# Kernel tuning notes

Measured on AMD Instinct MI355X. Metric: run time of the kernel, lower is better.

Reference implementation:

```python
import jax, jax.numpy as jnp
import numpy as np

B = 4096
T_STEPS = 2048


def setup_inputs() -> dict:
    key = jax.random.key(0)
    k1, k2, k3 = jax.random.split(key, 3)
    inputs = jax.random.normal(k1, (B, T_STEPS), dtype=jnp.float32)
    # replicate torch init: params = rand(t); params /= sum(|params|); alternate signs
    p = jax.random.uniform(k2, (T_STEPS,), dtype=jnp.float32)
    p = p / jnp.sum(jnp.abs(p))
    sign = jnp.where(jnp.arange(T_STEPS) % 2 == 0, jnp.float32(1.0), jnp.float32(-1.0))
    params = p * sign
    bias = jax.random.normal(k3, (1,), dtype=jnp.float32)
    return {"inputs": inputs, "params": params, "bias": bias}


def reference(inputs, params, bias):
    """AR(t) recurrence: for i in [t, 2t): x_i = sum_j x_{i-1-j} * params[j] + bias.
    inputs: [B, t] seed values; returns the t generated values per row, [B, t].
    """
    t_steps = params.shape[0]
    # torch.dot uses inputs reversed (newest first) against params, so the
    # window kept in oldest->newest order pairs with reversed params.
    p_rev = params[::-1]

    def step(window, _):
        # window: [B, t] last t values, oldest -> newest
        new = window @ p_rev + bias[0]  # [B]
        window = jnp.concatenate([window[:, 1:], new[:, None]], axis=1)
        return window, new

    _, outs = jax.lax.scan(step, inputs, None, length=t_steps)
    return outs.T  # [B, t_steps]
```

## Files before the change

kernel.cpp:

```cpp
#include <hip/hip_runtime.h>
#include <hip/hip_bf16.h>

typedef _Float16 f16;
typedef _Float16 f16x8 __attribute__((ext_vector_type(8)));
typedef float f32x4 __attribute__((ext_vector_type(4)));

constexpr int TS = 2048;
constexpr int BB = 4096;

__device__ __forceinline__ int swz4(int c) { return c ^ ((c >> 3) & 7); }

struct ToepShared { char Xs[16384]; char Ws[8192]; };

union MegaShared {
  ToepShared t;
  struct {
    float rp1[2048];
    float h[2048];
    float hist[1024];
    float hbuf[2052];
  } hb;
};

template <bool REV>
__device__ void toep_body(ToepShared& lds, int w, const f16* __restrict__ Xg,
                          const char* __restrict__ Wg,
                          const float* __restrict__ biasp, void* __restrict__ Yg) {
  char* Xs = lds.Xs;
  char* Ws = lds.Ws;
  const int tid = threadIdx.x;
  const int lane = tid & 63;
  const int wid = tid >> 6;
  const int wrow = (wid >> 1) * 64;
  const int wcol = (wid & 1) * 32;
  const int px = w & 15;
  const int b0 = (w >> 4) * 128;

  float binit = 0.0f;
  if (REV) binit = biasp[0];

  for (int phase = 0; phase < 2; ++phase) {
    const int mblk = phase ? (31 - px) : px;
    const int m0 = mblk * 64;
    const int k0b = REV ? m0 : 0;
    const int k0e = REV ? TS : (m0 + 64);

    f32x4 acc[4][2];
    #pragma unroll
    for (int i = 0; i < 4; ++i)
      #pragma unroll
      for (int j = 0; j < 2; ++j) acc[i][j] = {binit, binit, binit, binit};

    for (int k0 = k0b; k0 < k0e; k0 += 64) {
      __syncthreads();
      #pragma unroll
      for (int t2 = 0; t2 < 4; ++t2) {
        const int t = wid * 4 + t2;
        const int row = t * 8 + (lane >> 3);
        const char* src = (const char*)Xg + ((size_t)(b0 + row) * TS + k0) * 2
                          + (((lane & 7) * 16) ^ ((row & 7) << 4));
        __builtin_amdgcn_global_load_lds(
            (const __attribute__((address_space(1))) unsigned int*)src,
            (__attribute__((address_space(3))) unsigned int*)(Xs + t * 1024),
            16, 0, 0);
      }
      const int dlt = (REV ? (k0 - m0) : (m0 - k0)) >> 6;
      const char* wsrc = Wg + (size_t)dlt * 8192;
      #pragma unroll
      for (int p = 0; p < 2; ++p) {
        const int t = wid * 2 + p;
        __builtin_amdgcn_global_load_lds(
            (const __attribute__((address_space(1))) unsigned int*)(wsrc + t * 1024 + lane * 16),
            (__attribute__((address_space(3))) unsigned int*)(Ws + t * 1024),
            16, 0, 0);
      }
      __syncthreads();

      #pragma unroll
      for (int ks = 0; ks < 2; ++ks) {
        const int colb = ks * 64 + ((lane >> 4) * 16);
        f16x8 af[4], bf[2];
        #pragma unroll
        for (int i = 0; i < 4; ++i) {
          const int row = wrow + i * 16 + (lane & 15);
          af[i] = *(const f16x8*)(Xs + row * 128 + (colb ^ ((row & 7) << 4)));
        }
        #pragma unroll
        for (int j = 0; j < 2; ++j) {
          const int n = wcol + j * 16 + (lane & 15);
          bf[j] = *(const f16x8*)(Ws + n * 128 + (colb ^ ((n & 7) << 4)));
        }
        #pragma unroll
        for (int i = 0; i < 4; ++i)
          #pragma unroll
          for (int j = 0; j < 2; ++j)
            acc[i][j] = __builtin_amdgcn_mfma_f32_16x16x32_f16(
                af[i], bf[j], acc[i][j], 0, 0, 0);
      }
    }

    #pragma unroll
    for (int i = 0; i < 4; ++i) {
      #pragma unroll
      for (int j = 0; j < 2; ++j) {
        #pragma unroll
        for (int r = 0; r < 4; ++r) {
          const int row = b0 + wrow + i * 16 + (lane >> 4) * 4 + r;
          const int col = m0 + wcol + j * 16 + (lane & 15);
          if (REV)
            ((f16*)Yg)[(size_t)row * TS + col] = (f16)acc[i][j][r];
          else
            ((float*)Yg)[(size_t)row * TS + col] = acc[i][j][r];
        }
      }
    }
  }
}

__device__ void h_block_body(MegaShared& lds, const float* __restrict__ params,
                             char* __restrict__ WgC) {
  float* rp1 = lds.hb.rp1;
  float* h_s = lds.hb.h;
  float* hist = lds.hb.hist;
  float* hb = lds.hb.hbuf;

  const int tid = threadIdx.x;
  const int lane = tid & 63;
  const int wave = tid >> 6;

  for (int c = tid; c < 512; c += 256) {
    const int y = c * 4;
    f32x4 v;
    v[0] = params[2046 - y];
    v[1] = params[2045 - y];
    v[2] = params[2044 - y];
    v[3] = (y + 3 < 2047) ? params[2043 - y] : 0.0f;
    *(f32x4*)&rp1[swz4(c) * 4] = v;
  }
  __syncthreads();

  if (wave == 0) {
    float hv = (lane == 0) ? 1.0f : 0.0f;
    for (int m = 1; m < 32; ++m) {
      float partial = 0.0f;
      if (lane < m) {
        const int yi = 2047 - m + lane;
        partial = hv * rp1[swz4(yi >> 2) * 4 + (yi & 3)];
      }
      #pragma unroll
      for (int off = 32; off; off >>= 1) partial += __shfl_xor(partial, off);
      if (lane == m) hv = partial;
    }
    if (lane < 32) h_s[lane] = hv;
  }
  __syncthreads();

  const int sub = tid & 7;
  const int g0 = tid >> 3;

  for (int n = 32; n < 2048; n <<= 1) {
    const int ng16 = n >> 4;
    const int T = (n >= 128) ? (n >> 7) : 1;

    for (int gi = g0; gi < ng16; gi += 32) {
      float acc[16];
      #pragma unroll
      for (int j = 0; j < 16; ++j) acc[j] = 0.0f;
      const int ybase = (2047 - n) - gi * 16 - 15;
      for (int t = 0; t < T; ++t) {
        const int m16 = (sub + 8 * t) * 16;
        if (m16 < n) {
          const int c0 = (ybase + m16) >> 2;
          f32x4 wv[8];
          #pragma unroll
          for (int q = 0; q < 8; ++q) wv[q] = *(const f32x4*)&rp1[swz4(c0 + q) * 4];
          f32x4 hv4[4];
          #pragma unroll
          for (int q = 0; q < 4; ++q) hv4[q] = *(const f32x4*)&h_s[m16 + 4 * q];
          #pragma unroll
          for (int d = 0; d < 16; ++d) {
            const float hd = hv4[d >> 2][d & 3];
            #pragma unroll
            for (int j = 0; j < 16; ++j) {
              const int k = d - j + 15;
              acc[j] += hd * wv[k >> 2][k & 3];
            }
          }
        }
      }
      #pragma unroll
      for (int j = 0; j < 16; ++j) {
        acc[j] += __shfl_xor(acc[j], 1);
        acc[j] += __shfl_xor(acc[j], 2);
        acc[j] += __shfl_xor(acc[j], 4);
      }
      if (sub == 0) {
        #pragma unroll
        for (int q = 0; q < 4; ++q) {
          f32x4 v = {acc[4 * q], acc[4 * q + 1], acc[4 * q + 2], acc[4 * q + 3]};
          *(f32x4*)&hist[gi * 16 + 4 * q] = v;
        }
      }
    }
    __syncthreads();

    const int P = n + 3;
    const int nchunk = (2 * n + 4) >> 2;
    for (int c = tid; c < nchunk; c += 256) {
      f32x4 v;
      #pragma unroll
      for (int q = 0; q < 4; ++q) {
        const int idx = 4 * c + q - P;
        v[q] = ((unsigned)idx < (unsigned)n) ? hist[idx] : 0.0f;
      }
      *(f32x4*)&hb[swz4(c) * 4] = v;
    }
    __syncthreads();

    for (int gi = g0; gi < ng16; gi += 32) {
      float acc[16];
      #pragma unroll
      for (int j = 0; j < 16; ++j) acc[j] = 0.0f;
      int t_end = (gi >= sub) ? (((gi - sub) >> 3) + 1) : 0;
      if (t_end > T) t_end = T;
      const int ybase = P + gi * 16 - 15;
      for (int t = 0; t < t_end; ++t) {
        const int r16 = (sub + 8 * t) * 16;
        const int c0 = (ybase - r16) >> 2;
        f32x4 wv[8];
        #pragma unroll
        for (int q = 0; q < 8; ++q) wv[q] = *(const f32x4*)&hb[swz4(c0 + q) * 4];
        f32x4 hv4[4];
        #pragma unroll
        for (int q = 0; q < 4; ++q) hv4[q] = *(const f32x4*)&h_s[r16 + 4 * q];
        #pragma unroll
        for (int d = 0; d < 16; ++d) {
          const float hd = hv4[d >> 2][d & 3];
          #pragma unroll
          for (int j = 0; j < 16; ++j) {
            const int k = j - d + 15;
            acc[j] += hd * wv[k >> 2][k & 3];
          }
        }
      }
      #pragma unroll
      for (int j = 0; j < 16; ++j) {
        acc[j] += __shfl_xor(acc[j], 1);
        acc[j] += __shfl_xor(acc[j], 2);
        acc[j] += __shfl_xor(acc[j], 4);
      }
      if (sub == 0) {
        #pragma unroll
        for (int q = 0; q < 4; ++q) {
          f32x4 v = {acc[4 * q], acc[4 * q + 1], acc[4 * q + 2], acc[4 * q + 3]};
          *(f32x4*)&h_s[n + gi * 16 + 4 * q] = v;
        }
      }
    }
    __syncthreads();
  }

  const int n2 = tid >> 2, kq = tid & 3;
  for (int dlt = 0; dlt < 32; ++dlt) {
    char* tile = WgC + (size_t)dlt * 8192;
    #pragma unroll
    for (int part = 0; part < 2; ++part) {
      const int k8 = kq * 16 + part * 8;
      f16x8 v;
      #pragma unroll
      for (int ii = 0; ii < 8; ++ii) {
        const int k = k8 + ii;
        const int dd = dlt * 64 + n2 - k;
        v[ii] = ((unsigned)dd < (unsigned)TS) ? (f16)h_s[dd] : (f16)0.0f;
      }
      *(f16x8*)(tile + n2 * 128 + ((2 * k8) ^ ((n2 & 7) << 4))) = v;
    }
  }
}

__global__ __launch_bounds__(256) void conv_prep(
    const float* __restrict__ X, f16* __restrict__ Xh,
    const float* __restrict__ params, char* __restrict__ Wg) {
  const int b = blockIdx.x;
  const int tid = threadIdx.x;
  if (b < 2048) {
    const size_t base = ((size_t)b * 256 + tid) * 16;
    const float4 a0 = *(const float4*)&X[base];
    const float4 a1 = *(const float4*)&X[base + 4];
    const float4 a2 = *(const float4*)&X[base + 8];
    const float4 a3 = *(const float4*)&X[base + 12];
    f16x8 v0 = {(f16)a0.x, (f16)a0.y, (f16)a0.z, (f16)a0.w,
                (f16)a1.x, (f16)a1.y, (f16)a1.z, (f16)a1.w};
    f16x8 v1 = {(f16)a2.x, (f16)a2.y, (f16)a2.z, (f16)a2.w,
                (f16)a3.x, (f16)a3.y, (f16)a3.z, (f16)a3.w};
    *(f16x8*)&Xh[base] = v0;
    *(f16x8*)&Xh[base + 8] = v1;
  } else {
    const int dlt = b - 2048;
    char* tile = Wg + (size_t)dlt * 8192;
    const int n = tid >> 2, kq = tid & 3;
    #pragma unroll
    for (int part = 0; part < 2; ++part) {
      const int k8 = kq * 16 + part * 8;
      f16x8 v;
      #pragma unroll
      for (int ii = 0; ii < 8; ++ii) {
        const int k = k8 + ii;
        const int dd = dlt * 64 + k - n;
        v[ii] = ((unsigned)dd < (unsigned)TS) ? (f16)params[2047 - dd] : (f16)0.0f;
      }
      *(f16x8*)(tile + n * 128 + ((2 * k8) ^ ((n & 7) << 4))) = v;
    }
  }
}

__global__ __launch_bounds__(256, 2) void mega_A(
    const f16* __restrict__ Xh, char* __restrict__ Wg,
    const float* __restrict__ biasp, f16* __restrict__ u,
    const float* __restrict__ params) {
  __shared__ MegaShared lds;
  const int b = blockIdx.x;
  if (b == 512) {
    h_block_body(lds, params, Wg + 32 * 8192);
    return;
  }
  toep_body<true>(lds.t, (b & 7) * 64 + (b >> 3), Xh, Wg, biasp, (void*)u);
}

__global__ __launch_bounds__(256, 2) void toep_C(
    const f16* __restrict__ u, const char* __restrict__ WgC,
    float* __restrict__ out) {
  __shared__ ToepShared lds;
  const int b = blockIdx.x;
  toep_body<false>(lds, (b & 7) * 64 + (b >> 3), u, WgC, nullptr, (void*)out);
}

extern "C" void kernel_launch(void* const* d_in, const int* in_sizes, int n_in,
                              void* d_out, int out_size, void* d_ws, size_t ws_size,
                              hipStream_t stream) {
  const float* inputs = (const float*)d_in[0];
  const float* params = (const float*)d_in[1];
  const float* bias   = (const float*)d_in[2];
  float* out = (float*)d_out;

  char* ws = (char*)d_ws;
  f16*  Xh = (f16*)ws;
  f16*  u  = (f16*)(ws + (size_t)BB * TS * 2);
  char* Wg = ws + (size_t)BB * TS * 4;

  conv_prep<<<2080, 256, 0, stream>>>(inputs, Xh, params, Wg);
  mega_A<<<513, 256, 0, stream>>>(Xh, Wg, bias, u, params);
  toep_C<<<512, 256, 0, stream>>>(u, Wg + 32 * 8192, out);
}
```

Before: 118.2 us.

## Move impulse-response block into prep kernel and halve per-thread output tile

The serial impulse-response (h) computation block moves from the first Toeplitz GEMM kernel into the conversion/prep kernel as block 0, so its long serial chain overlaps the bandwidth-bound fp32-to-fp16 conversion instead of extending the GEMM kernel's tail. The GEMM kernel no longer carries the large union shared-memory footprint. Inside the h block, each thread group now produces 8 outputs instead of 16, doubling the groups to spread work across more threads, and the h/hist arrays use swizzled LDS indexing to reduce bank conflicts. The cost is a prep kernel with a large static LDS allocation and launch bounds of 1, which may lower occupancy for the conversion blocks.

```diff
diff --git a/kernel.cpp b/kernel.cpp
--- a/kernel.cpp
+++ b/kernel.cpp
@@ -12,14 +12,11 @@
 
 struct ToepShared { char Xs[16384]; char Ws[8192]; };
 
-union MegaShared {
-  ToepShared t;
-  struct {
-    float rp1[2048];
-    float h[2048];
-    float hist[1024];
-    float hbuf[2052];
-  } hb;
+struct HShared {
+  float rp1[2048];
+  float h[2048];
+  float hist[1024];
+  float hbuf[2052];
 };
 
 template <bool REV>
@@ -117,12 +114,12 @@
   }
 }
 
-__device__ void h_block_body(MegaShared& lds, const float* __restrict__ params,
+__device__ void h_block_body(HShared& S, const float* __restrict__ params,
                              char* __restrict__ WgC) {
-  float* rp1 = lds.hb.rp1;
-  float* h_s = lds.hb.h;
-  float* hist = lds.hb.hist;
-  float* hb = lds.hb.hbuf;
+  float* rp1 = S.rp1;
+  float* h_s = S.h;
+  float* hist = S.hist;
+  float* hb = S.hbuf;
 
   const int tid = threadIdx.x;
   const int lane = tid & 63;
@@ -159,47 +156,46 @@
   const int g0 = tid >> 3;
 
   for (int n = 32; n < 2048; n <<= 1) {
-    const int ng16 = n >> 4;
+    const int ngrp = n >> 3;
     const int T = (n >= 128) ? (n >> 7) : 1;
 
-    for (int gi = g0; gi < ng16; gi += 32) {
-      float acc[16];
-      #pragma unroll
-      for (int j = 0; j < 16; ++j) acc[j] = 0.0f;
-      const int ybase = (2047 - n) - gi * 16 - 15;
+    for (int gi = g0; gi < ngrp; gi += 32) {
+      float acc[8];
+      #pragma unroll
+      for (int j = 0; j < 8; ++j) acc[j] = 0.0f;
+      const int cb = 510 - (n >> 2) - 2 * gi;
       for (int t = 0; t < T; ++t) {
-        const int m16 = (sub + 8 * t) * 16;
-        if (m16 < n) {
-          const int c0 = (ybase + m16) >> 2;
-          f32x4 wv[8];
-          #pragma unroll
-          for (int q = 0; q < 8; ++q) wv[q] = *(const f32x4*)&rp1[swz4(c0 + q) * 4];
+        const int mb = sub + 8 * t;
+        if (16 * mb < n) {
+          const int c0 = cb + 4 * mb;
+          f32x4 wv[6];
+          #pragma unroll
+          for (int q = 0; q < 6; ++q) wv[q] = *(const f32x4*)&rp1[swz4(c0 + q) * 4];
           f32x4 hv4[4];
           #pragma unroll
-          for (int q = 0; q < 4; ++q) hv4[q] = *(const f32x4*)&h_s[m16 + 4 * q];
+          for (int q = 0; q < 4; ++q) hv4[q] = *(const f32x4*)&h_s[swz4(4 * mb + q) * 4];
           #pragma unroll
           for (int d = 0; d < 16; ++d) {
             const float hd = hv4[d >> 2][d & 3];
             #pragma unroll
-            for (int j = 0; j < 16; ++j) {
-              const int k = d - j + 15;
+            for (int j = 0; j < 8; ++j) {
+              const int k = d - j + 7;
               acc[j] += hd * wv[k >> 2][k & 3];
             }
           }
         }
       }
       #pragma unroll
-      for (int j = 0; j < 16; ++j) {
+      for (int j = 0; j < 8; ++j) {
         acc[j] += __shfl_xor(acc[j], 1);
         acc[j] += __shfl_xor(acc[j], 2);
         acc[j] += __shfl_xor(acc[j], 4);
       }
       if (sub == 0) {
-        #pragma unroll
-        for (int q = 0; q < 4; ++q) {
-          f32x4 v = {acc[4 * q], acc[4 * q + 1], acc[4 * q + 2], acc[4 * q + 3]};
-          *(f32x4*)&hist[gi * 16 + 4 * q] = v;
-        }
+        f32x4 lo = {acc[0], acc[1], acc[2], acc[3]};
+        f32x4 hi = {acc[4], acc[5], acc[6], acc[7]};
+        *(f32x4*)&hist[swz4(2 * gi) * 4] = lo;
+        *(f32x4*)&hist[swz4(2 * gi + 1) * 4] = hi;
       }
     }
     __syncthreads();
@@ -211,50 +207,52 @@
       #pragma unroll
       for (int q = 0; q < 4; ++q) {
         const int idx = 4 * c + q - P;
-        v[q] = ((unsigned)idx < (unsigned)n) ? hist[idx] : 0.0f;
+        v[q] = ((unsigned)idx < (unsigned)n)
+                   ? hist[swz4(idx >> 2) * 4 + (idx & 3)] : 0.0f;
       }
       *(f32x4*)&hb[swz4(c) * 4] = v;
     }
     __syncthreads();
 
-    for (int gi = g0; gi < ng16; gi += 32) {
-      float acc[16];
-      #pragma unroll
-      for (int j = 0; j < 16; ++j) acc[j] = 0.0f;
-      int t_end = (gi >= sub) ? (((gi - sub) >> 3) + 1) : 0;
+    for (int gi = g0; gi < ngrp; gi += 32) {
+      float acc[8];
+      #pragma unroll
+      for (int j = 0; j < 8; ++j) acc[j] = 0.0f;
+      const int cb = ((n - 12) >> 2) + 2 * gi;
+      const int G = (8 * gi + 7) >> 4;
+      int t_end = (G >= sub) ? (((G - sub) >> 3) + 1) : 0;
       if (t_end > T) t_end = T;
-      const int ybase = P + gi * 16 - 15;
       for (int t = 0; t < t_end; ++t) {
-        const int r16 = (sub + 8 * t) * 16;
-        const int c0 = (ybase - r16) >> 2;
-        f32x4 wv[8];
-        #pragma unroll
-        for (int q = 0; q < 8; ++q) wv[q] = *(const f32x4*)&hb[swz4(c0 + q) * 4];
+        const int rb = sub + 8 * t;
+        const int c0 = cb - 4 * rb;
+        f32x4 wv[6];
+        #pragma unroll
+        for (int q = 0; q < 6; ++q) wv[q] = *(const f32x4*)&hb[swz4(c0 + q) * 4];
         f32x4 hv4[4];
         #pragma unroll
-        for (int q = 0; q < 4; ++q) hv4[q] = *(const f32x4*)&h_s[r16 + 4 * q];
+        for (int q = 0; q < 4; ++q) hv4[q] = *(const f32x4*)&h_s[swz4(4 * rb + q) * 4];
         #pragma unroll
         for (int d = 0; d < 16; ++d) {
           const float hd = hv4[d >> 2][d & 3];
           #pragma unroll
-          for (int j = 0; j < 16; ++j) {
+          for (int j = 0; j < 8; ++j) {
             const int k = j - d + 15;
             acc[j] += hd * wv[k >> 2][k & 3];
           }
         }
       }
       #pragma unroll
-      for (int j = 0; j < 16; ++j) {
+      for (int j = 0; j < 8; ++j) {
         acc[j] += __shfl_xor(acc[j], 1);
         acc[j] += __shfl_xor(acc[j], 2);
         acc[j] += __shfl_xor(acc[j], 4);
       }
       if (sub == 0) {
-        #pragma unroll
-        for (int q = 0; q < 4; ++q) {
-          f32x4 v = {acc[4 * q], acc[4 * q + 1], acc[4 * q + 2], acc[4 * q + 3]};
-          *(f32x4*)&h_s[n + gi * 16 + 4 * q] = v;
-        }
+        f32x4 lo = {acc[0], acc[1], acc[2], acc[3]};
+        f32x4 hi = {acc[4], acc[5], acc[6], acc[7]};
+        const int cw = (n >> 2) + 2 * gi;
+        *(f32x4*)&h_s[swz4(cw) * 4] = lo;
+        *(f32x4*)&h_s[swz4(cw + 1) * 4] = hi;
       }
     }
     __syncthreads();
@@ -271,32 +269,27 @@
       for (int ii = 0; ii < 8; ++ii) {
         const int k = k8 + ii;
         const int dd = dlt * 64 + n2 - k;
-        v[ii] = ((unsigned)dd < (unsigned)TS) ? (f16)h_s[dd] : (f16)0.0f;
+        v[ii] = ((unsigned)dd < (unsigned)TS)
+                    ? (f16)h_s[swz4(dd >> 2) * 4 + (dd & 3)] : (f16)0.0f;
       }
       *(f16x8*)(tile + n2 * 128 + ((2 * k8) ^ ((n2 & 7) << 4))) = v;
     }
   }
 }
 
-__global__ __launch_bounds__(256) void conv_prep(
+__global__ __launch_bounds__(256, 1) void conv_prep(
     const float* __restrict__ X, f16* __restrict__ Xh,
     const float* __restrict__ params, char* __restrict__ Wg) {
+  __shared__ HShared S;
   const int b = blockIdx.x;
   const int tid = threadIdx.x;
-  if (b < 2048) {
-    const size_t base = ((size_t)b * 256 + tid) * 16;
-    const float4 a0 = *(const float4*)&X[base];
-    const float4 a1 = *(const float4*)&X[base + 4];
-    const float4 a2 = *(const float4*)&X[base + 8];
-    const float4 a3 = *(const float4*)&X[base + 12];
-    f16x8 v0 = {(f16)a0.x, (f16)a0.y, (f16)a0.z, (f16)a0.w,
-                (f16)a1.x, (f16)a1.y, (f16)a1.z, (f16)a1.w};
-    f16x8 v1 = {(f16)a2.x, (f16)a2.y, (f16)a2.z, (f16)a2.w,
-                (f16)a3.x, (f16)a3.y, (f16)a3.z, (f16)a3.w};
-    *(f16x8*)&Xh[base] = v0;
-    *(f16x8*)&Xh[base + 8] = v1;
-  } else {
-    const int dlt = b - 2048;
+
+  if (b == 0) {
+    h_block_body(S, params, Wg + 32 * 8192);
+    return;
+  }
+  if (b <= 32) {
+    const int dlt = b - 1;
     char* tile = Wg + (size_t)dlt * 8192;
     const int n = tid >> 2, kq = tid & 3;
     #pragma unroll
@@ -311,20 +304,27 @@
       }
       *(f16x8*)(tile + n * 128 + ((2 * k8) ^ ((n & 7) << 4))) = v;
     }
-  }
-}
-
-__global__ __launch_bounds__(256, 2) void mega_A(
-    const f16* __restrict__ Xh, char* __restrict__ Wg,
-    const float* __restrict__ biasp, f16* __restrict__ u,
-    const float* __restrict__ params) {
-  __shared__ MegaShared lds;
+    return;
+  }
+  const size_t base = ((size_t)(b - 33) * 256 + tid) * 16;
+  const float4 a0 = *(const float4*)&X[base];
+  const float4 a1 = *(const float4*)&X[base + 4];
+  const float4 a2 = *(const float4*)&X[base + 8];
+  const float4 a3 = *(const float4*)&X[base + 12];
+  f16x8 v0 = {(f16)a0.x, (f16)a0.y, (f16)a0.z, (f16)a0.w,
+              (f16)a1.x, (f16)a1.y, (f16)a1.z, (f16)a1.w};
+  f16x8 v1 = {(f16)a2.x, (f16)a2.y, (f16)a2.z, (f16)a2.w,
+              (f16)a3.x, (f16)a3.y, (f16)a3.z, (f16)a3.w};
+  *(f16x8*)&Xh[base] = v0;
+  *(f16x8*)&Xh[base + 8] = v1;
+}
+
+__global__ __launch_bounds__(256, 2) void toep_A(
+    const f16* __restrict__ Xh, const char* __restrict__ Wg,
+    const float* __restrict__ biasp, f16* __restrict__ u) {
+  __shared__ ToepShared lds;
   const int b = blockIdx.x;
-  if (b == 512) {
-    h_block_body(lds, params, Wg + 32 * 8192);
-    return;
-  }
-  toep_body<true>(lds.t, (b & 7) * 64 + (b >> 3), Xh, Wg, biasp, (void*)u);
+  toep_body<true>(lds, (b & 7) * 64 + (b >> 3), Xh, Wg, biasp, (void*)u);
 }
 
 __global__ __launch_bounds__(256, 2) void toep_C(
@@ -348,7 +348,7 @@
   f16*  u  = (f16*)(ws + (size_t)BB * TS * 2);
   char* Wg = ws + (size_t)BB * TS * 4;
 
-  conv_prep<<<2080, 256, 0, stream>>>(inputs, Xh, params, Wg);
-  mega_A<<<513, 256, 0, stream>>>(Xh, Wg, bias, u, params);
+  conv_prep<<<2081, 256, 0, stream>>>(inputs, Xh, params, Wg);
+  toep_A<<<512, 256, 0, stream>>>(Xh, Wg, bias, u);
   toep_C<<<512, 256, 0, stream>>>(u, Wg + 32 * 8192, out);
 }
```

Result: slower. 139.0 us (+17.7%).
